# Performance work log

Measured on AMD Instinct MI355X. Metric: run time of the kernel, lower is better.

The kernel has to match this reference:

```python
import jax, jax.numpy as jnp
import numpy as np
import math

EMB_DIM = 1024
NUM_HEADS = 16
D_H = EMB_DIM // NUM_HEADS
B, S = 2, 2048


def setup_inputs() -> dict:
    key = jax.random.key(0)
    ks = jax.random.split(key, 6)
    limit = math.sqrt(6.0 / (EMB_DIM + D_H))  # xavier_uniform per head
    x = jax.random.normal(ks[0], (B, S, EMB_DIM), dtype=jnp.float32)
    Wq = jax.random.uniform(ks[1], (NUM_HEADS, EMB_DIM, D_H), jnp.float32, -limit, limit)
    Wk = jax.random.uniform(ks[2], (NUM_HEADS, EMB_DIM, D_H), jnp.float32, -limit, limit)
    Wv = jax.random.uniform(ks[3], (NUM_HEADS, EMB_DIM, D_H), jnp.float32, -limit, limit)
    bq = jnp.zeros((NUM_HEADS, D_H), jnp.float32)
    bk = jnp.zeros((NUM_HEADS, D_H), jnp.float32)
    bv = jnp.zeros((NUM_HEADS, D_H), jnp.float32)
    limo = math.sqrt(6.0 / (EMB_DIM + EMB_DIM))
    W_O = jax.random.uniform(ks[4], (EMB_DIM, EMB_DIM), jnp.float32, -limo, limo)
    causal_mask = jnp.tril(jnp.ones((S, S), jnp.float32))
    padding_mask = jnp.zeros((B, S), jnp.bool_)  # all-False: nothing padded
    return {"x": x, "Wq": Wq, "bq": bq, "Wk": Wk, "bk": bk, "Wv": Wv,
            "bv": bv, "W_O": W_O, "causal_mask": causal_mask,
            "padding_mask": padding_mask}


def reference(x, Wq, bq, Wk, bk, Wv, bv, W_O, causal_mask, padding_mask):
    # Per-head projections, vectorized over heads: [B,S,E] x [H,E,D] -> [B,H,S,D]
    Q = jnp.einsum('bse,hed->bhsd', x, Wq) + bq[None, :, None, :]
    K = jnp.einsum('bse,hed->bhsd', x, Wk) + bk[None, :, None, :]
    V = jnp.einsum('bse,hed->bhsd', x, Wv) + bv[None, :, None, :]
    scores = jnp.einsum('bhsd,bhtd->bhst', Q, K) / math.sqrt(D_H)
    neg_inf = jnp.float32(-jnp.inf)
    scores = jnp.where(causal_mask[None, None, :, :] == 0, neg_inf, scores)
    scores = jnp.where(padding_mask[:, None, None, :], neg_inf, scores)
    attn = jax.nn.softmax(scores, axis=-1)
    out = jnp.einsum('bhst,bhtd->bhsd', attn, V)  # [B,H,S,D]
    # concat heads in order (dim=-1) -> [B,S,H*D]
    x_concat = out.transpose(0, 2, 1, 3).reshape(B, S, EMB_DIM)
    return x_concat @ W_O
```

## Files before the change

### kernel.cpp

```cpp
#include <hip/hip_runtime.h>
#include <hip/hip_bf16.h>


typedef __hip_bfloat16 bf16;
typedef __attribute__((ext_vector_type(8))) short bfrag;
typedef __attribute__((ext_vector_type(4))) float f32x4;
typedef __attribute__((ext_vector_type(16))) float f32x16;
typedef __attribute__((ext_vector_type(4))) short short4v;

#define MFMA16(a, b, c) __builtin_amdgcn_mfma_f32_16x16x32_bf16(a, b, c, 0, 0, 0)
#define MFMA32(a, b, c) __builtin_amdgcn_mfma_f32_32x32x16_bf16(a, b, c, 0, 0, 0)

__device__ __forceinline__ void gl_lds16(const bf16* g, bf16* l) {
  __builtin_amdgcn_global_load_lds(
      (const __attribute__((address_space(1))) void*)g,
      (__attribute__((address_space(3))) void*)l, 16, 0, 0);
}

__global__ __launch_bounds__(256) void cast_f32_bf16(const float* __restrict__ src,
                                                     bf16* __restrict__ dst, int n) {
  int i = (blockIdx.x * 256 + threadIdx.x) * 8;
  if (i >= n) return;
  float4 a = *(const float4*)(src + i);
  float4 b = *(const float4*)(src + i + 4);
  union { bf16 h[8]; bfrag v; } tmp;
  tmp.h[0] = __float2bfloat16(a.x); tmp.h[1] = __float2bfloat16(a.y);
  tmp.h[2] = __float2bfloat16(a.z); tmp.h[3] = __float2bfloat16(a.w);
  tmp.h[4] = __float2bfloat16(b.x); tmp.h[5] = __float2bfloat16(b.y);
  tmp.h[6] = __float2bfloat16(b.z); tmp.h[7] = __float2bfloat16(b.w);
  *(bfrag*)(dst + i) = tmp.v;
}

__global__ __launch_bounds__(256) void transpose_w(const float* __restrict__ src,
                                                   bf16* __restrict__ dst,
                                                   int R, int C) {
  __shared__ bf16 tile[64][80];
  int c0 = blockIdx.x * 64, r0 = blockIdx.y * 64;
  int t = threadIdx.x;
  int lr = t >> 3, lc = (t & 7) << 3;
#pragma unroll
  for (int p = 0; p < 2; ++p) {
    int r = lr + p * 32;
    const float* s = src + (long)(r0 + r) * C + c0 + lc;
    union { bf16 h[8]; bfrag v; } tmp;
#pragma unroll
    for (int j = 0; j < 8; ++j) tmp.h[j] = __float2bfloat16(s[j]);
    *(bfrag*)(&tile[r][lc]) = tmp.v;
  }
  __syncthreads();
#pragma unroll
  for (int p = 0; p < 2; ++p) {
    int c = lr + p * 32;
    union { bf16 h[8]; bfrag v; } tmp;
#pragma unroll
    for (int j = 0; j < 8; ++j) tmp.h[j] = tile[lc + j][c];
    *(bfrag*)(dst + (long)(c0 + c) * R + r0 + lc) = tmp.v;
  }
}

__global__ __launch_bounds__(256) void transpose_qkv(const float* __restrict__ Wq,
                                                     const float* __restrict__ Wk,
                                                     const float* __restrict__ Wv,
                                                     bf16* __restrict__ dst) {
  __shared__ bf16 tile[64][80];
  int z = blockIdx.z;
  int w = z >> 4, h = z & 15;
  const float* src = ((w == 0) ? Wq : (w == 1) ? Wk : Wv) + (long)h * 1024 * 64;
  bf16* d = dst + ((long)w * 1024 + h * 64) * 1024;
  int r0 = blockIdx.y * 64;
  int t = threadIdx.x;
  int lr = t >> 3, lc = (t & 7) << 3;
#pragma unroll
  for (int p = 0; p < 2; ++p) {
    int r = lr + p * 32;
    const float* s = src + (long)(r0 + r) * 64 + lc;
    union { bf16 h8[8]; bfrag v; } tmp;
#pragma unroll
    for (int j = 0; j < 8; ++j) tmp.h8[j] = __float2bfloat16(s[j]);
    *(bfrag*)(&tile[r][lc]) = tmp.v;
  }
  __syncthreads();
#pragma unroll
  for (int p = 0; p < 2; ++p) {
    int c = lr + p * 32;
    union { bf16 h8[8]; bfrag v; } tmp;
#pragma unroll
    for (int j = 0; j < 8; ++j) tmp.h8[j] = tile[lc + j][c];
    *(bfrag*)(d + (long)c * 1024 + r0 + lc) = tmp.v;
  }
}

__global__ __launch_bounds__(256) void gemm_qkv128(const bf16* __restrict__ xb,
                                                   const bf16* __restrict__ WT,
                                                   const float* __restrict__ bq,
                                                   const float* __restrict__ bk,
                                                   const float* __restrict__ bv,
                                                   bf16* __restrict__ Q,
                                                   bf16* __restrict__ K_,
                                                   bf16* __restrict__ Vt) {
  const int K = 1024;
  __shared__ bf16 As[128][32];
  __shared__ bf16 Bs[128][32];
  int n0 = blockIdx.x * 128;
  int m0 = blockIdx.y * 128;
  int t = threadIdx.x, wave = t >> 6, lane = t & 63, quad = lane >> 4, col = lane & 15;
  int wr = (wave >> 1) * 64, wc = (wave & 1) * 64;
  f32x4 acc[4][4] = {};

  int srow = 32 * wave + (lane >> 2);
  int sg = (lane & 3) * 8;
  const bf16* Ag = xb + (long)(m0 + srow) * K + sg;
  const bf16* Bg = WT + (long)(n0 + srow) * K + sg;

  for (int k0 = 0; k0 < K; k0 += 32) {
    __syncthreads();
    gl_lds16(Ag + k0, &As[srow][sg]);
    gl_lds16(Ag + 16 * K + k0, &As[srow + 16][sg]);
    gl_lds16(Bg + k0, &Bs[srow][sg]);
    gl_lds16(Bg + 16 * K + k0, &Bs[srow + 16][sg]);
    __syncthreads();
    bfrag ra[4], rb[4];
#pragma unroll
    for (int i = 0; i < 4; ++i) ra[i] = *(const bfrag*)(&As[wr + 16 * i + col][quad * 8]);
#pragma unroll
    for (int c = 0; c < 4; ++c) rb[c] = *(const bfrag*)(&Bs[wc + 16 * c + col][quad * 8]);
#pragma unroll
    for (int c = 0; c < 4; ++c)
#pragma unroll
      for (int i = 0; i < 4; ++i) acc[c][i] = MFMA16(ra[i], rb[c], acc[c][i]);
  }

  int sel = n0 >> 10;
  const float* bias = (sel == 0) ? bq : (sel == 1) ? bk : bv;
#pragma unroll
  for (int c = 0; c < 4; ++c) {
    int n = n0 + wc + 16 * c + col;
    int nn = n & 1023;
    float bvv = bias[nn];
#pragma unroll
    for (int i = 0; i < 4; ++i) {
      int mb = m0 + wr + 16 * i + quad * 4;
      if (sel < 2) {
        bf16* dst = (sel == 0) ? Q : K_;
#pragma unroll
        for (int r = 0; r < 4; ++r)
          dst[(long)(mb + r) * 1024 + nn] = __float2bfloat16(acc[c][i][r] + bvv);
      } else {
        int b = mb >> 11, s0 = mb & 2047;
        int h = nn >> 6, d = nn & 63;
        union { bf16 h4[4]; short4v v; } pk;
#pragma unroll
        for (int r = 0; r < 4; ++r) pk.h4[r] = __float2bfloat16(acc[c][i][r] + bvv);
        *(short4v*)(Vt + (long)(((b << 4) + h) * 64 + d) * 2048 + s0) = pk.v;
      }
    }
  }
}

__global__ __launch_bounds__(256) void gemm_out(const bf16* __restrict__ A,
                                                const bf16* __restrict__ Bt,
                                                float* __restrict__ Cf) {
  const int K = 1024;
  __shared__ bf16 As[128][32];
  __shared__ bf16 Bs[64][32];
  int n0 = blockIdx.x * 64;
  int m0 = blockIdx.y * 128;
  int t = threadIdx.x;
  int wave = t >> 6, lane = t & 63, quad = lane >> 4, col = lane & 15;
  int wr = (wave >> 1) * 64, wc = (wave & 1) * 32;
  f32x4 acc[2][4] = {};

  int srA = 32 * wave + (lane >> 2);
  int srB = 16 * wave + (lane >> 2);
  int sg = (lane & 3) * 8;
  const bf16* Ag0 = A + (long)(m0 + srA) * K + sg;
  const bf16* Ag1 = A + (long)(m0 + srA + 16) * K + sg;
  const bf16* Bg = Bt + (long)(n0 + srB) * K + sg;

  for (int k0 = 0; k0 < K; k0 += 32) {
    __syncthreads();
    gl_lds16(Ag0 + k0, &As[srA][sg]);
    gl_lds16(Ag1 + k0, &As[srA + 16][sg]);
    gl_lds16(Bg + k0, &Bs[srB][sg]);
    __syncthreads();
    bfrag ra[4], rb[2];
#pragma unroll
    for (int i = 0; i < 4; ++i) ra[i] = *(const bfrag*)(&As[wr + 16 * i + col][quad * 8]);
#pragma unroll
    for (int c = 0; c < 2; ++c) rb[c] = *(const bfrag*)(&Bs[wc + 16 * c + col][quad * 8]);
#pragma unroll
    for (int c = 0; c < 2; ++c)
#pragma unroll
      for (int i = 0; i < 4; ++i) acc[c][i] = MFMA16(ra[i], rb[c], acc[c][i]);
  }

#pragma unroll
  for (int c = 0; c < 2; ++c) {
    int n = n0 + wc + 16 * c + col;
#pragma unroll
    for (int i = 0; i < 4; ++i)
#pragma unroll
      for (int r = 0; r < 4; ++r) {
        int m = m0 + wr + 16 * i + quad * 4 + r;
        Cf[(long)m * 1024 + n] = acc[c][i][r];
      }
  }
}

__global__ __launch_bounds__(256) void attn_kernel(const bf16* __restrict__ Qc,
                                                   const bf16* __restrict__ Kc,
                                                   const bf16* __restrict__ Vt,
                                                   bf16* __restrict__ O) {
  int pair = blockIdx.x;
  int bh = blockIdx.y;
  int b = bh >> 4, h = bh & 15;

  __shared__ bf16 Ks[128][72];
  __shared__ bf16 Vs[64][136];
  __shared__ bf16 Ps[64][136];

  int t = threadIdx.x, wave = t >> 6, lane = t & 63;
  int qh = wave >> 1, jh = wave & 1, hi = lane >> 5, l5 = lane & 31;

  const float SC = 0.125f;
  const float SH = 11.0903549f;

  int krow = t >> 3, kg = (t & 7) * 8;
  int vrow = t >> 4, vg = (t & 15) * 8;
  const bf16* Kbase = Kc + (long)(b * 2048 + krow) * 1024 + h * 64 + kg;
  const bf16* Vbase = Vt + (long)(bh * 64 + vrow) * 2048 + vg;

#pragma unroll
  for (int qsel = 0; qsel < 2; ++qsel) {
    int qt = qsel ? (31 - pair) : pair;
    int q0 = qt * 64;
    int nj = (qt >> 1) + 1;

    bfrag qa[4];
    const bf16* qp = Qc + (long)(b * 2048 + q0 + 32 * qh + l5) * 1024 + h * 64 + hi * 8;
#pragma unroll
    for (int kd = 0; kd < 4; ++kd) qa[kd] = *(const bfrag*)(qp + kd * 16);

    f32x16 o0, o1;
    float lsum[16];
#pragma unroll
    for (int r = 0; r < 16; ++r) { o0[r] = 0.f; o1[r] = 0.f; lsum[r] = 0.f; }

    bfrag kreg[4], vreg[4];
#pragma unroll
    for (int i = 0; i < 4; ++i)
      kreg[i] = *(const bfrag*)(Kbase + (long)(32 * i) * 1024);

    for (int jt = 0; jt < nj; ++jt) {
      int j0 = jt * 128;
      __syncthreads();
#pragma unroll
      for (int i = 0; i < 4; ++i)
        *(bfrag*)(&Ks[krow + 32 * i][kg]) = kreg[i];
      int jn = (jt + 1 < nj) ? (jt + 1) * 128 : jt * 128;
#pragma unroll
      for (int i = 0; i < 4; ++i)
        vreg[i] = *(const bfrag*)(Vbase + (long)(16 * i) * 2048 + j0);
#pragma unroll
      for (int i = 0; i < 4; ++i)
        kreg[i] = *(const bfrag*)(Kbase + (long)(jn + 32 * i) * 1024);
      __syncthreads();

      f32x16 s0, s1;
#pragma unroll
      for (int r = 0; r < 16; ++r) { s0[r] = 0.f; s1[r] = 0.f; }
#pragma unroll
      for (int kd = 0; kd < 4; ++kd) {
        bfrag kb0 = *(const bfrag*)(&Ks[jh * 64 + l5][kd * 16 + hi * 8]);
        bfrag kb1 = *(const bfrag*)(&Ks[jh * 64 + 32 + l5][kd * 16 + hi * 8]);
        s0 = MFMA32(qa[kd], kb0, s0);
        s1 = MFMA32(qa[kd], kb1, s1);
      }

      bool lastT = (jt == nj - 1);
#pragma unroll
      for (int jb = 0; jb < 2; ++jb) {
        int j = j0 + jh * 64 + jb * 32 + l5;
#pragma unroll
        for (int r = 0; r < 16; ++r) {
          int qrow = (r & 3) + 8 * (r >> 2) + 4 * hi;
          float sv = jb ? s1[r] : s0[r];
          float p = __expf(fmaf(sv, SC, -SH));
          if (lastT) p = (j <= q0 + 32 * qh + qrow) ? p : 0.f;
          lsum[r] += p;
          Ps[32 * qh + qrow][jh * 64 + jb * 32 + l5] = __float2bfloat16(p);
        }
      }
#pragma unroll
      for (int i = 0; i < 4; ++i)
        *(bfrag*)(&Vs[vrow + 16 * i][vg]) = vreg[i];
      __syncthreads();

#pragma unroll
      for (int kj = 0; kj < 4; ++kj) {
        bfrag pa = *(const bfrag*)(&Ps[32 * qh + l5][jh * 64 + kj * 16 + hi * 8]);
        bfrag vb0 = *(const bfrag*)(&Vs[l5][jh * 64 + kj * 16 + hi * 8]);
        bfrag vb1 = *(const bfrag*)(&Vs[32 + l5][jh * 64 + kj * 16 + hi * 8]);
        o0 = MFMA32(pa, vb0, o0);
        o1 = MFMA32(pa, vb1, o1);
      }
    }

#pragma unroll
    for (int off = 1; off < 32; off <<= 1)
#pragma unroll
      for (int r = 0; r < 16; ++r) lsum[r] += __shfl_xor(lsum[r], off, 64);

    __syncthreads();
    float* Osc = (float*)&Ps[0][0];
    float* Lsc = (float*)&Vs[0][0];
    if (jh == 1) {
#pragma unroll
      for (int r = 0; r < 16; ++r) {
        int qrow = (r & 3) + 8 * (r >> 2) + 4 * hi;
        Osc[(qh * 32 + qrow) * 68 + 0 * 32 + l5] = o0[r];
        Osc[(qh * 32 + qrow) * 68 + 1 * 32 + l5] = o1[r];
      }
      if (l5 == 0) {
#pragma unroll
        for (int r = 0; r < 16; ++r) {
          int qrow = (r & 3) + 8 * (r >> 2) + 4 * hi;
          Lsc[qh * 32 + qrow] = lsum[r];
        }
      }
    }
    __syncthreads();
    if (jh == 0) {
#pragma unroll
      for (int r = 0; r < 16; ++r) {
        int qrow = (r & 3) + 8 * (r >> 2) + 4 * hi;
        float inv = 1.f / (lsum[r] + Lsc[qh * 32 + qrow]);
        int iq = q0 + 32 * qh + qrow;
        float v0 = o0[r] + Osc[(qh * 32 + qrow) * 68 + 0 * 32 + l5];
        float v1 = o1[r] + Osc[(qh * 32 + qrow) * 68 + 1 * 32 + l5];
        O[(long)(b * 2048 + iq) * 1024 + h * 64 + l5] = __float2bfloat16(v0 * inv);
        O[(long)(b * 2048 + iq) * 1024 + h * 64 + 32 + l5] = __float2bfloat16(v1 * inv);
      }
    }
  }
}

extern "C" void kernel_launch(void* const* d_in, const int* in_sizes, int n_in,
                              void* d_out, int out_size, void* d_ws, size_t ws_size,
                              hipStream_t stream) {
  const float* x  = (const float*)d_in[0];
  const float* Wq = (const float*)d_in[1];
  const float* bq = (const float*)d_in[2];
  const float* Wk = (const float*)d_in[3];
  const float* bk = (const float*)d_in[4];
  const float* Wv = (const float*)d_in[5];
  const float* bv = (const float*)d_in[6];
  const float* Wo = (const float*)d_in[7];
  float* out = (float*)d_out;

  bf16* ws = (bf16*)d_ws;
  const long MB1 = 1 << 20;
  bf16* WqkvT = ws + 0 * MB1;
  bf16* WoT   = ws + 3 * MB1;
  bf16* Q     = ws + 4 * MB1;
  bf16* K_    = ws + 8 * MB1;
  bf16* Vt    = ws + 12 * MB1;
  bf16* O     = ws + 16 * MB1;
  bf16* xb    = ws + 20 * MB1;

  cast_f32_bf16<<<2048, 256, 0, stream>>>(x, xb, 4096 * 1024);
  transpose_qkv<<<dim3(1, 16, 48), 256, 0, stream>>>(Wq, Wk, Wv, WqkvT);
  transpose_w<<<dim3(16, 16, 1), 256, 0, stream>>>(Wo, WoT, 1024, 1024);

  gemm_qkv128<<<dim3(24, 32), 256, 0, stream>>>(xb, WqkvT, bq, bk, bv, Q, K_, Vt);

  attn_kernel<<<dim3(16, 32), 256, 0, stream>>>(Q, K_, Vt, O);

  gemm_out<<<dim3(16, 32), 256, 0, stream>>>(O, WoT, out);
}
```

Before: 215.5 us.

## Merge weight prep kernels, register-prefetch GEMM tiles, use exp2 softmax

Folds the two weight-transpose kernels into one launch. Both GEMMs drop direct global-to-LDS loads for register-staged prefetch of the next K=64 tile into padded LDS (row stride 72), halving barrier count per K and overlapping global loads with MFMA work. The attention softmax swaps __expf with a fixed shift for a hardware exp2 with a folded log2e scale. Costs are higher register pressure and extra LDS, which may lower occupancy.

```diff
diff --git a/kernel.cpp b/kernel.cpp
--- a/kernel.cpp
+++ b/kernel.cpp
@@ -10,12 +10,6 @@
 
 #define MFMA16(a, b, c) __builtin_amdgcn_mfma_f32_16x16x32_bf16(a, b, c, 0, 0, 0)
 #define MFMA32(a, b, c) __builtin_amdgcn_mfma_f32_32x32x16_bf16(a, b, c, 0, 0, 0)
-
-__device__ __forceinline__ void gl_lds16(const bf16* g, bf16* l) {
-  __builtin_amdgcn_global_load_lds(
-      (const __attribute__((address_space(1))) void*)g,
-      (__attribute__((address_space(3))) void*)l, 16, 0, 0);
-}
 
 __global__ __launch_bounds__(256) void cast_f32_bf16(const float* __restrict__ src,
                                                      bf16* __restrict__ dst, int n) {
@@ -31,49 +25,35 @@
   *(bfrag*)(dst + i) = tmp.v;
 }
 
-__global__ __launch_bounds__(256) void transpose_w(const float* __restrict__ src,
-                                                   bf16* __restrict__ dst,
-                                                   int R, int C) {
+__global__ __launch_bounds__(256) void prep_weights(const float* __restrict__ Wq,
+                                                    const float* __restrict__ Wk,
+                                                    const float* __restrict__ Wv,
+                                                    const float* __restrict__ Wo,
+                                                    bf16* __restrict__ WqkvT,
+                                                    bf16* __restrict__ WoT) {
   __shared__ bf16 tile[64][80];
-  int c0 = blockIdx.x * 64, r0 = blockIdx.y * 64;
+  int id = blockIdx.x;
+  const float* src;
+  bf16* dst;
+  int srcld, dstld, r0, c0;
+  if (id < 768) {
+    int w = id >> 8, h = (id >> 4) & 15;
+    r0 = (id & 15) * 64; c0 = 0;
+    src = ((w == 0) ? Wq : (w == 1) ? Wk : Wv) + (long)h * 1024 * 64;
+    dst = WqkvT + ((long)w * 1024 + h * 64) * 1024;
+    srcld = 64; dstld = 1024;
+  } else {
+    int j = id - 768;
+    c0 = (j & 15) * 64; r0 = (j >> 4) * 64;
+    src = Wo; dst = WoT;
+    srcld = 1024; dstld = 1024;
+  }
   int t = threadIdx.x;
   int lr = t >> 3, lc = (t & 7) << 3;
 #pragma unroll
   for (int p = 0; p < 2; ++p) {
     int r = lr + p * 32;
-    const float* s = src + (long)(r0 + r) * C + c0 + lc;
-    union { bf16 h[8]; bfrag v; } tmp;
-#pragma unroll
-    for (int j = 0; j < 8; ++j) tmp.h[j] = __float2bfloat16(s[j]);
-    *(bfrag*)(&tile[r][lc]) = tmp.v;
-  }
-  __syncthreads();
-#pragma unroll
-  for (int p = 0; p < 2; ++p) {
-    int c = lr + p * 32;
-    union { bf16 h[8]; bfrag v; } tmp;
-#pragma unroll
-    for (int j = 0; j < 8; ++j) tmp.h[j] = tile[lc + j][c];
-    *(bfrag*)(dst + (long)(c0 + c) * R + r0 + lc) = tmp.v;
-  }
-}
-
-__global__ __launch_bounds__(256) void transpose_qkv(const float* __restrict__ Wq,
-                                                     const float* __restrict__ Wk,
-                                                     const float* __restrict__ Wv,
-                                                     bf16* __restrict__ dst) {
-  __shared__ bf16 tile[64][80];
-  int z = blockIdx.z;
-  int w = z >> 4, h = z & 15;
-  const float* src = ((w == 0) ? Wq : (w == 1) ? Wk : Wv) + (long)h * 1024 * 64;
-  bf16* d = dst + ((long)w * 1024 + h * 64) * 1024;
-  int r0 = blockIdx.y * 64;
-  int t = threadIdx.x;
-  int lr = t >> 3, lc = (t & 7) << 3;
-#pragma unroll
-  for (int p = 0; p < 2; ++p) {
-    int r = lr + p * 32;
-    const float* s = src + (long)(r0 + r) * 64 + lc;
+    const float* s = src + (long)(r0 + r) * srcld + c0 + lc;
     union { bf16 h8[8]; bfrag v; } tmp;
 #pragma unroll
     for (int j = 0; j < 8; ++j) tmp.h8[j] = __float2bfloat16(s[j]);
@@ -86,7 +66,7 @@
     union { bf16 h8[8]; bfrag v; } tmp;
 #pragma unroll
     for (int j = 0; j < 8; ++j) tmp.h8[j] = tile[lc + j][c];
-    *(bfrag*)(d + (long)c * 1024 + r0 + lc) = tmp.v;
+    *(bfrag*)(dst + (long)(c0 + c) * dstld + r0 + lc) = tmp.v;
   }
 }
 
@@ -99,35 +79,53 @@
                                                    bf16* __restrict__ K_,
                                                    bf16* __restrict__ Vt) {
   const int K = 1024;
-  __shared__ bf16 As[128][32];
-  __shared__ bf16 Bs[128][32];
+  __shared__ bf16 As[128][72];
+  __shared__ bf16 Bs[128][72];
   int n0 = blockIdx.x * 128;
   int m0 = blockIdx.y * 128;
   int t = threadIdx.x, wave = t >> 6, lane = t & 63, quad = lane >> 4, col = lane & 15;
   int wr = (wave >> 1) * 64, wc = (wave & 1) * 64;
   f32x4 acc[4][4] = {};
 
-  int srow = 32 * wave + (lane >> 2);
-  int sg = (lane & 3) * 8;
-  const bf16* Ag = xb + (long)(m0 + srow) * K + sg;
-  const bf16* Bg = WT + (long)(n0 + srow) * K + sg;
-
-  for (int k0 = 0; k0 < K; k0 += 32) {
-    __syncthreads();
-    gl_lds16(Ag + k0, &As[srow][sg]);
-    gl_lds16(Ag + 16 * K + k0, &As[srow + 16][sg]);
-    gl_lds16(Bg + k0, &Bs[srow][sg]);
-    gl_lds16(Bg + 16 * K + k0, &Bs[srow + 16][sg]);
-    __syncthreads();
-    bfrag ra[4], rb[4];
-#pragma unroll
-    for (int i = 0; i < 4; ++i) ra[i] = *(const bfrag*)(&As[wr + 16 * i + col][quad * 8]);
-#pragma unroll
-    for (int c = 0; c < 4; ++c) rb[c] = *(const bfrag*)(&Bs[wc + 16 * c + col][quad * 8]);
-#pragma unroll
-    for (int c = 0; c < 4; ++c)
-#pragma unroll
-      for (int i = 0; i < 4; ++i) acc[c][i] = MFMA16(ra[i], rb[c], acc[c][i]);
+  int srow = t >> 1, scol = (t & 1) * 32;
+  const bf16* Ag = xb + (long)(m0 + srow) * K + scol;
+  const bf16* Bg = WT + (long)(n0 + srow) * K + scol;
+
+  bfrag Ar[4], Br[4];
+#pragma unroll
+  for (int i = 0; i < 4; ++i) {
+    Ar[i] = *(const bfrag*)(Ag + 8 * i);
+    Br[i] = *(const bfrag*)(Bg + 8 * i);
+  }
+
+  for (int k0 = 0; k0 < K; k0 += 64) {
+    __syncthreads();
+#pragma unroll
+    for (int i = 0; i < 4; ++i) {
+      *(bfrag*)(&As[srow][scol + 8 * i]) = Ar[i];
+      *(bfrag*)(&Bs[srow][scol + 8 * i]) = Br[i];
+    }
+    int kn = (k0 + 64 < K) ? k0 + 64 : k0;
+#pragma unroll
+    for (int i = 0; i < 4; ++i) {
+      Ar[i] = *(const bfrag*)(Ag + kn + 8 * i);
+      Br[i] = *(const bfrag*)(Bg + kn + 8 * i);
+    }
+    __syncthreads();
+#pragma unroll
+    for (int kc = 0; kc < 2; ++kc) {
+      bfrag ra[4], rb[4];
+#pragma unroll
+      for (int i = 0; i < 4; ++i)
+        ra[i] = *(const bfrag*)(&As[wr + 16 * i + col][kc * 32 + quad * 8]);
+#pragma unroll
+      for (int c = 0; c < 4; ++c)
+        rb[c] = *(const bfrag*)(&Bs[wc + 16 * c + col][kc * 32 + quad * 8]);
+#pragma unroll
+      for (int c = 0; c < 4; ++c)
+#pragma unroll
+        for (int i = 0; i < 4; ++i) acc[c][i] = MFMA16(ra[i], rb[c], acc[c][i]);
+    }
   }
 
   int sel = n0 >> 10;
@@ -161,8 +159,8 @@
                                                 const bf16* __restrict__ Bt,
                                                 float* __restrict__ Cf) {
   const int K = 1024;
-  __shared__ bf16 As[128][32];
-  __shared__ bf16 Bs[64][32];
+  __shared__ bf16 As[128][72];
+  __shared__ bf16 Bs[64][72];
   int n0 = blockIdx.x * 64;
   int m0 = blockIdx.y * 128;
   int t = threadIdx.x;
@@ -170,28 +168,43 @@
   int wr = (wave >> 1) * 64, wc = (wave & 1) * 32;
   f32x4 acc[2][4] = {};
 
-  int srA = 32 * wave + (lane >> 2);
-  int srB = 16 * wave + (lane >> 2);
-  int sg = (lane & 3) * 8;
-  const bf16* Ag0 = A + (long)(m0 + srA) * K + sg;
-  const bf16* Ag1 = A + (long)(m0 + srA + 16) * K + sg;
-  const bf16* Bg = Bt + (long)(n0 + srB) * K + sg;
-
-  for (int k0 = 0; k0 < K; k0 += 32) {
-    __syncthreads();
-    gl_lds16(Ag0 + k0, &As[srA][sg]);
-    gl_lds16(Ag1 + k0, &As[srA + 16][sg]);
-    gl_lds16(Bg + k0, &Bs[srB][sg]);
-    __syncthreads();
-    bfrag ra[4], rb[2];
-#pragma unroll
-    for (int i = 0; i < 4; ++i) ra[i] = *(const bfrag*)(&As[wr + 16 * i + col][quad * 8]);
-#pragma unroll
-    for (int c = 0; c < 2; ++c) rb[c] = *(const bfrag*)(&Bs[wc + 16 * c + col][quad * 8]);
-#pragma unroll
-    for (int c = 0; c < 2; ++c)
-#pragma unroll
-      for (int i = 0; i < 4; ++i) acc[c][i] = MFMA16(ra[i], rb[c], acc[c][i]);
+  int srA = t >> 1, scA = (t & 1) * 32;
+  int srB = t >> 2, scB = (t & 3) * 16;
+  const bf16* Ag = A + (long)(m0 + srA) * K + scA;
+  const bf16* Bg = Bt + (long)(n0 + srB) * K + scB;
+
+  bfrag Ar[4], Br[2];
+#pragma unroll
+  for (int i = 0; i < 4; ++i) Ar[i] = *(const bfrag*)(Ag + 8 * i);
+#pragma unroll
+  for (int i = 0; i < 2; ++i) Br[i] = *(const bfrag*)(Bg + 8 * i);
+
+  for (int k0 = 0; k0 < K; k0 += 64) {
+    __syncthreads();
+#pragma unroll
+    for (int i = 0; i < 4; ++i) *(bfrag*)(&As[srA][scA + 8 * i]) = Ar[i];
+#pragma unroll
+    for (int i = 0; i < 2; ++i) *(bfrag*)(&Bs[srB][scB + 8 * i]) = Br[i];
+    int kn = (k0 + 64 < K) ? k0 + 64 : k0;
+#pragma unroll
+    for (int i = 0; i < 4; ++i) Ar[i] = *(const bfrag*)(Ag + kn + 8 * i);
+#pragma unroll
+    for (int i = 0; i < 2; ++i) Br[i] = *(const bfrag*)(Bg + kn + 8 * i);
+    __syncthreads();
+#pragma unroll
+    for (int kc = 0; kc < 2; ++kc) {
+      bfrag ra[4], rb[2];
+#pragma unroll
+      for (int i = 0; i < 4; ++i)
+        ra[i] = *(const bfrag*)(&As[wr + 16 * i + col][kc * 32 + quad * 8]);
+#pragma unroll
+      for (int c = 0; c < 2; ++c)
+        rb[c] = *(const bfrag*)(&Bs[wc + 16 * c + col][kc * 32 + quad * 8]);
+#pragma unroll
+      for (int c = 0; c < 2; ++c)
+#pragma unroll
+        for (int i = 0; i < 4; ++i) acc[c][i] = MFMA16(ra[i], rb[c], acc[c][i]);
+    }
   }
 
 #pragma unroll
@@ -222,8 +235,7 @@
   int t = threadIdx.x, wave = t >> 6, lane = t & 63;
   int qh = wave >> 1, jh = wave & 1, hi = lane >> 5, l5 = lane & 31;
 
-  const float SC = 0.125f;
-  const float SH = 11.0903549f;
+  const float SC2 = 0.18033688f;
 
   int krow = t >> 3, kg = (t & 7) * 8;
   int vrow = t >> 4, vg = (t & 15) * 8;
@@ -285,7 +297,7 @@
         for (int r = 0; r < 16; ++r) {
           int qrow = (r & 3) + 8 * (r >> 2) + 4 * hi;
           float sv = jb ? s1[r] : s0[r];
-          float p = __expf(fmaf(sv, SC, -SH));
+          float p = __builtin_amdgcn_exp2f(fmaf(sv, SC2, -16.0f));
           if (lastT) p = (j <= q0 + 32 * qh + qrow) ? p : 0.f;
           lsum[r] += p;
           Ps[32 * qh + qrow][jh * 64 + jb * 32 + l5] = __float2bfloat16(p);
@@ -369,8 +381,7 @@
   bf16* xb    = ws + 20 * MB1;
 
   cast_f32_bf16<<<2048, 256, 0, stream>>>(x, xb, 4096 * 1024);
-  transpose_qkv<<<dim3(1, 16, 48), 256, 0, stream>>>(Wq, Wk, Wv, WqkvT);
-  transpose_w<<<dim3(16, 16, 1), 256, 0, stream>>>(Wo, WoT, 1024, 1024);
+  prep_weights<<<1024, 256, 0, stream>>>(Wq, Wk, Wv, Wo, WqkvT, WoT);
 
   gemm_qkv128<<<dim3(24, 32), 256, 0, stream>>>(xb, WqkvT, bq, bk, bv, Q, K_, Vt);
 
```

New measurement: 212.2 us. No clear change (-1.5%).
